# Performance work log

Hardware: AMD Instinct MI355X
Metric: run time of the kernel (lower is better)

Reference implementation:

```python
import jax, jax.numpy as jnp
import numpy as np

B, T, D = 32, 2000, 1024

def setup_inputs() -> dict:
    key = jax.random.key(0)
    # drive with positive mean current so neurons actually spike
    I_seq = 100.0 * jax.random.normal(key, (B, T, D), dtype=jnp.float32) + 250.0
    C, g_L, E_L, V_T, Delta_T, tau_w = 200.0, 10.0, -70.0, -50.0, 2.0, 120.0
    a, b, R, V_reset, V_spike, dt = 0.0, 0.0, 1.0, -65.0, 30.0, 0.1
    tau_m = C / max(1e-06, g_L)
    params = jnp.array([tau_m, E_L, V_T, Delta_T, R, tau_w, a, b, V_reset, V_spike, dt],
                       dtype=jnp.float32)
    return {"I_seq": I_seq, "params": params}


def reference(I_seq, params):
    tau_m, E_L, V_T, Delta_T, R, tau_w, a, b, V_reset, V_spike, dt = params
    Bs, Ts, Ds = I_seq.shape
    # flatten to (T, B*D): scan over time, all neurons vectorized
    flat_I = jnp.transpose(I_seq, (1, 0, 2)).reshape(Ts, Bs * Ds)
    V0 = jnp.full((Bs * Ds,), E_L, dtype=I_seq.dtype)
    w0 = jnp.zeros((Bs * Ds,), dtype=I_seq.dtype)

    def step(carry, i_t):
        V, w = carry
        exp_term = Delta_T * jnp.exp((V - V_T) / Delta_T)
        dV = (-(V - E_L) + exp_term - R * w + R * i_t) / tau_m
        V = V + dt * dV
        dw = (a * (V - E_L) - w) / tau_w
        w = w + dt * dw
        spk = (V >= V_spike).astype(V.dtype)
        V = jnp.where(spk > 0.0, V_reset, V)
        w = jnp.where(spk > 0.0, w + b, w)
        return (V, w), spk

    (_, _), spikes = jax.lax.scan(step, (V0, w0), flat_I)  # spikes: (T, B*D)
    return jnp.transpose(spikes.reshape(Ts, Bs, Ds), (1, 0, 2))  # (B, T, D)
```

## Files before the change

### kernel.cpp

```cpp
#include <hip/hip_runtime.h>


#define Bn 32
#define Tn 2000
#define Dn 1024
#define NEUR (Bn * Dn)
#define UNR 16
#define NB (Tn / UNR)

#define EXP_LOG2EF 1.44269504088896341f
#define EXP_C1 0.693359375f
#define EXP_C2 -2.12194440e-4f
#define EXP_P0 1.9875691500e-4f
#define EXP_P1 1.3981999507e-3f
#define EXP_P2 8.3334519073e-3f
#define EXP_P3 4.1665795894e-2f
#define EXP_P4 1.6666665459e-1f
#define EXP_P5 5.0000001201e-1f

__device__ __forceinline__ float ref_expf(float x) {
    #pragma clang fp contract(off)
    float fx = __builtin_floorf(__builtin_fmaf(x, EXP_LOG2EF, 0.5f));
    float xr = __builtin_fmaf(fx, -EXP_C1, x);
    xr = __builtin_fmaf(fx, -EXP_C2, xr);
    float z2 = xr * xr;
    float y = EXP_P0;
    y = __builtin_fmaf(y, xr, EXP_P1);
    y = __builtin_fmaf(y, xr, EXP_P2);
    y = __builtin_fmaf(y, xr, EXP_P3);
    y = __builtin_fmaf(y, xr, EXP_P4);
    y = __builtin_fmaf(y, xr, EXP_P5);
    y = __builtin_fmaf(y, z2, xr);
    y = y + 1.0f;
    const int n = (int)fx;
    return y * __int_as_float((n + 127) << 23);
}

__device__ __forceinline__ float ref_expf_scaled(float x, int kdt) {
    #pragma clang fp contract(off)
    float fx = __builtin_floorf(__builtin_fmaf(x, EXP_LOG2EF, 0.5f));
    float xr = __builtin_fmaf(fx, -EXP_C1, x);
    xr = __builtin_fmaf(fx, -EXP_C2, xr);
    float z2 = xr * xr;
    float y = EXP_P0;
    y = __builtin_fmaf(y, xr, EXP_P1);
    y = __builtin_fmaf(y, xr, EXP_P2);
    y = __builtin_fmaf(y, xr, EXP_P3);
    y = __builtin_fmaf(y, xr, EXP_P4);
    y = __builtin_fmaf(y, xr, EXP_P5);
    y = __builtin_fmaf(y, z2, xr);
    y = y + 1.0f;
    const int n = (int)fx;
    return y * __int_as_float((n + 127 + kdt) << 23);
}

__device__ __forceinline__ float div_uniform(float x, float d, float r) {
    #pragma clang fp contract(off)
    float q = x * r;
    float e = __builtin_fmaf(-d, q, x);
    return __builtin_fmaf(e, r, q);
}

__device__ __forceinline__ void step_simple(float& V, float i_t, float& spk_out,
                                            float E_L, float V_T, float Delta_T,
                                            float R, float tau_m, float V_spike,
                                            float V_reset, float dt) {
    #pragma clang fp contract(off)
    const float e  = ref_expf((V - V_T) / Delta_T);
    const float et = Delta_T * e;
    float nm = (-(V - E_L) + et);
    nm = nm + R * i_t;
    const float dV = nm / tau_m;
    V = __builtin_fmaf(dt, dV, V);
    spk_out = (V >= V_spike) ? 1.0f : 0.0f;
    V = (V >= V_spike) ? V_reset : V;
}

__device__ __forceinline__ void step_general(float& V, float& w, float i_t, float& spk_out,
                                             float E_L, float V_T, float Delta_T,
                                             float R, float tau_m, float tau_w,
                                             float a, float b,
                                             float V_spike, float V_reset, float dt) {
    #pragma clang fp contract(off)
    const float e  = ref_expf((V - V_T) / Delta_T);
    const float et = Delta_T * e;
    float nm = (-(V - E_L) + et);
    nm = __builtin_fmaf(-R, w, nm);
    nm = __builtin_fmaf(R, i_t, nm);
    const float dV = nm / tau_m;
    V = __builtin_fmaf(dt, dV, V);
    const float dwn = __builtin_fmaf(a, (V - E_L), -w);
    const float dw  = dwn / tau_w;
    w = __builtin_fmaf(dt, dw, w);
    spk_out = (V >= V_spike) ? 1.0f : 0.0f;
    const bool s = (V >= V_spike);
    V = s ? V_reset : V;
    w = s ? (w + b) : w;
}

__launch_bounds__(128, 1)
__global__ void adex_kernel(const float* __restrict__ I,
                            const float* __restrict__ params,
                            float* __restrict__ out) {
    #pragma clang fp contract(off)

    const float tau_m   = params[0];
    const float E_L     = params[1];
    const float V_T     = params[2];
    const float Delta_T = params[3];
    const float R       = params[4];
    const float tau_w   = params[5];
    const float a       = params[6];
    const float b       = params[7];
    const float V_reset = params[8];
    const float V_spike = params[9];
    const float dt      = params[10];

    const int n = blockIdx.x * blockDim.x + threadIdx.x;
    if (n >= NEUR) return;
    const int bb = n >> 10;
    const int dd = n & (Dn - 1);

    const float* Ip = I   + (size_t)bb * (size_t)(Tn * Dn) + dd;
    float*       Op = out + (size_t)bb * (size_t)(Tn * Dn) + dd;

    float V = E_L;
    float bufA[UNR], bufB[UNR];

    #pragma unroll
    for (int k = 0; k < UNR; ++k) bufA[k] = Ip[k * Dn];

    const unsigned dtBits = __float_as_uint(Delta_T);
    const bool dtPow2 = ((dtBits & 0x7FFFFFu) == 0u) && Delta_T > 0.0f;
    const bool hot = (a == 0.0f) && (b == 0.0f) && (R == 1.0f) && dtPow2;

    if (hot) {
        const int   kdt = (int)((dtBits >> 23) & 0xFFu) - 127;
        const float rDT = 1.0f / Delta_T;
        const float rTM = 1.0f / tau_m;
        const float xC = (V_reset - V_T) * rDT;
        const float nC = E_L - V_reset;

        float x   = (V - V_T) * rDT;
        float nEL = E_L - V;

        for (int tb = 0; tb < NB; tb += 2) {
            if (tb + 1 < NB) {
                const float* p = Ip + (size_t)(tb + 1) * (UNR * Dn);
                #pragma unroll
                for (int k = 0; k < UNR; ++k) bufB[k] = p[k * Dn];
            }
            {
                float* o = Op + (size_t)tb * (UNR * Dn);
                #pragma unroll
                for (int k = 0; k < UNR; ++k) {
                    const float et = ref_expf_scaled(x, kdt);
                    float nm = nEL + et;
                    nm = nm + bufA[k];
                    const float dV = div_uniform(nm, tau_m, rTM);
                    const float Vr = __builtin_fmaf(dt, dV, V);
                    const bool  s  = (Vr >= V_spike);
                    o[k * Dn] = s ? 1.0f : 0.0f;
                    const float xn = (Vr - V_T) * rDT;
                    const float nn = E_L - Vr;
                    V   = s ? V_reset : Vr;
                    x   = s ? xC : xn;
                    nEL = s ? nC : nn;
                }
            }
            if (tb + 2 < NB) {
                const float* p = Ip + (size_t)(tb + 2) * (UNR * Dn);
                #pragma unroll
                for (int k = 0; k < UNR; ++k) bufA[k] = p[k * Dn];
            }
            if (tb + 1 < NB) {
                float* o = Op + (size_t)(tb + 1) * (UNR * Dn);
                #pragma unroll
                for (int k = 0; k < UNR; ++k) {
                    const float et = ref_expf_scaled(x, kdt);
                    float nm = nEL + et;
                    nm = nm + bufB[k];
                    const float dV = div_uniform(nm, tau_m, rTM);
                    const float Vr = __builtin_fmaf(dt, dV, V);
                    const bool  s  = (Vr >= V_spike);
                    o[k * Dn] = s ? 1.0f : 0.0f;
                    const float xn = (Vr - V_T) * rDT;
                    const float nn = E_L - Vr;
                    V   = s ? V_reset : Vr;
                    x   = s ? xC : xn;
                    nEL = s ? nC : nn;
                }
            }
        }
        return;
    }

    float w = 0.0f;
    const bool simple = (a == 0.0f) && (b == 0.0f);

    if (simple) {
        for (int tb = 0; tb < NB; tb += 2) {
            if (tb + 1 < NB) {
                const float* p = Ip + (size_t)(tb + 1) * (UNR * Dn);
                #pragma unroll
                for (int k = 0; k < UNR; ++k) bufB[k] = p[k * Dn];
            }
            {
                float* o = Op + (size_t)tb * (UNR * Dn);
                #pragma unroll
                for (int k = 0; k < UNR; ++k) {
                    float spk;
                    step_simple(V, bufA[k], spk, E_L, V_T, Delta_T, R, tau_m,
                                V_spike, V_reset, dt);
                    o[k * Dn] = spk;
                }
            }
            if (tb + 2 < NB) {
                const float* p = Ip + (size_t)(tb + 2) * (UNR * Dn);
                #pragma unroll
                for (int k = 0; k < UNR; ++k) bufA[k] = p[k * Dn];
            }
            if (tb + 1 < NB) {
                float* o = Op + (size_t)(tb + 1) * (UNR * Dn);
                #pragma unroll
                for (int k = 0; k < UNR; ++k) {
                    float spk;
                    step_simple(V, bufB[k], spk, E_L, V_T, Delta_T, R, tau_m,
                                V_spike, V_reset, dt);
                    o[k * Dn] = spk;
                }
            }
        }
    } else {
        for (int tb = 0; tb < NB; tb += 2) {
            if (tb + 1 < NB) {
                const float* p = Ip + (size_t)(tb + 1) * (UNR * Dn);
                #pragma unroll
                for (int k = 0; k < UNR; ++k) bufB[k] = p[k * Dn];
            }
            {
                float* o = Op + (size_t)tb * (UNR * Dn);
                #pragma unroll
                for (int k = 0; k < UNR; ++k) {
                    float spk;
                    step_general(V, w, bufA[k], spk, E_L, V_T, Delta_T, R, tau_m,
                                 tau_w, a, b, V_spike, V_reset, dt);
                    o[k * Dn] = spk;
                }
            }
            if (tb + 2 < NB) {
                const float* p = Ip + (size_t)(tb + 2) * (UNR * Dn);
                #pragma unroll
                for (int k = 0; k < UNR; ++k) bufA[k] = p[k * Dn];
            }
            if (tb + 1 < NB) {
                float* o = Op + (size_t)(tb + 1) * (UNR * Dn);
                #pragma unroll
                for (int k = 0; k < UNR; ++k) {
                    float spk;
                    step_general(V, w, bufB[k], spk, E_L, V_T, Delta_T, R, tau_m,
                                 tau_w, a, b, V_spike, V_reset, dt);
                    o[k * Dn] = spk;
                }
            }
        }
    }
}

extern "C" void kernel_launch(void* const* d_in, const int* in_sizes, int n_in,
                              void* d_out, int out_size, void* d_ws, size_t ws_size,
                              hipStream_t stream) {
    const float* I      = (const float*)d_in[0];
    const float* params = (const float*)d_in[1];
    float*       out    = (float*)d_out;

    dim3 block(128);
    dim3 grid(NEUR / 128);
    adex_kernel<<<grid, block, 0, stream>>>(I, params, out);
}
```

Baseline: 187.7 us.

## Split time axis into chunks with warm-up state convergence and sequential fixup

Splits the 2000-step scan into 5 time chunks run in parallel. Each later chunk starts from a bracket of possible membrane voltages and runs a 160-step warm-up to check whether every trajectory has collapsed onto the reset state. If it has not, a flag is set and a second kernel reruns that chunk sequentially from the true carried voltage. The aim is to expose five times more parallelism than the 256 single-wave blocks provide. The cost is the warm-up recompute, an extra launch and workspace traffic. Correctness relies on a heuristic convergence bound (fixed slack constants), and the path is only used when the workspace is large enough.

```diff
diff --git a/kernel.cpp b/kernel.cpp
--- a/kernel.cpp
+++ b/kernel.cpp
@@ -6,7 +6,13 @@
 #define Dn 1024
 #define NEUR (Bn * Dn)
 #define UNR 16
-#define NB (Tn / UNR)
+#define NC 5
+#define CHK 400
+#define WARM 160
+#define CBLK (CHK / UNR)
+#define WBLK (WARM / UNR)
+#define FBLK (Tn / UNR)
+#define BPC (NEUR / 128)
 
 #define EXP_LOG2EF 1.44269504088896341f
 #define EXP_C1 0.693359375f
@@ -36,7 +42,7 @@
     return y * __int_as_float((n + 127) << 23);
 }
 
-__device__ __forceinline__ float ref_expf_scaled(float x, int kdt) {
+__device__ __forceinline__ float expsc(float x, int kdt) {
     #pragma clang fp contract(off)
     float fx = __builtin_floorf(__builtin_fmaf(x, EXP_LOG2EF, 0.5f));
     float xr = __builtin_fmaf(fx, -EXP_C1, x);
@@ -54,11 +60,44 @@
     return y * __int_as_float((n + 127 + kdt) << 23);
 }
 
-__device__ __forceinline__ float div_uniform(float x, float d, float r) {
+__device__ __forceinline__ float mark_div(float x, float d, float r) {
     #pragma clang fp contract(off)
     float q = x * r;
     float e = __builtin_fmaf(-d, q, x);
     return __builtin_fmaf(e, r, q);
+}
+
+struct HP {
+    float tau_m, E_L, V_T, rDT, rTM, dt, Vs, Vrst, xC, nC;
+    int kdt;
+};
+
+__device__ __forceinline__ bool hot_step(float& V, float& x, float& nEL,
+                                         float i_t, const HP p) {
+    #pragma clang fp contract(off)
+    const float et = expsc(x, p.kdt);
+    float nm = nEL + et;
+    nm = nm + i_t;
+    const float dV = mark_div(nm, p.tau_m, p.rTM);
+    const float Vp = __builtin_fmaf(p.dt, dV, V);
+    const bool s = (Vp >= p.Vs);
+    const float xn = (Vp - p.V_T) * p.rDT;
+    const float nn = p.E_L - Vp;
+    V   = s ? p.Vrst : Vp;
+    x   = s ? p.xC : xn;
+    nEL = s ? p.nC : nn;
+    return s;
+}
+
+__device__ __forceinline__ float fpre(float V, float i_t, const HP p) {
+    #pragma clang fp contract(off)
+    const float xx = (V - p.V_T) * p.rDT;
+    const float nn = p.E_L - V;
+    const float et = expsc(xx, p.kdt);
+    float nm = nn + et;
+    nm = nm + i_t;
+    const float dV = mark_div(nm, p.tau_m, p.rTM);
+    return __builtin_fmaf(p.dt, dV, V);
 }
 
 __device__ __forceinline__ void step_simple(float& V, float i_t, float& spk_out,
@@ -98,12 +137,45 @@
     w = s ? (w + b) : w;
 }
 
+#define RUN_BLOCKS(IPTR, OPTR, NBLK, ...) do {                                    \
+    float bufA_[UNR], bufB_[UNR];                                                 \
+    _Pragma("unroll") for (int k = 0; k < UNR; ++k) bufA_[k] = (IPTR)[k * Dn];    \
+    for (int tb = 0; tb < (NBLK); tb += 2) {                                      \
+        if (tb + 1 < (NBLK)) {                                                    \
+            const float* pp_ = (IPTR) + (size_t)(tb + 1) * (UNR * Dn);            \
+            _Pragma("unroll") for (int k = 0; k < UNR; ++k) bufB_[k] = pp_[k*Dn]; \
+        }                                                                         \
+        {                                                                         \
+            float* oo_ = (OPTR) + (size_t)tb * (UNR * Dn);                        \
+            _Pragma("unroll") for (int k = 0; k < UNR; ++k) {                     \
+                const float i_t = bufA_[k];                                       \
+                float* OSLOT = oo_ + (size_t)k * Dn; (void)OSLOT;                 \
+                __VA_ARGS__;                                                      \
+            }                                                                     \
+        }                                                                         \
+        if (tb + 2 < (NBLK)) {                                                    \
+            const float* pp_ = (IPTR) + (size_t)(tb + 2) * (UNR * Dn);            \
+            _Pragma("unroll") for (int k = 0; k < UNR; ++k) bufA_[k] = pp_[k*Dn]; \
+        }                                                                         \
+        if (tb + 1 < (NBLK)) {                                                    \
+            float* oo_ = (OPTR) + (size_t)(tb + 1) * (UNR * Dn);                  \
+            _Pragma("unroll") for (int k = 0; k < UNR; ++k) {                     \
+                const float i_t = bufB_[k];                                       \
+                float* OSLOT = oo_ + (size_t)k * Dn; (void)OSLOT;                 \
+                __VA_ARGS__;                                                      \
+            }                                                                     \
+        }                                                                         \
+    }                                                                             \
+} while (0)
+
 __launch_bounds__(128, 1)
-__global__ void adex_kernel(const float* __restrict__ I,
-                            const float* __restrict__ params,
-                            float* __restrict__ out) {
-    #pragma clang fp contract(off)
-
+__global__ void adex_chunked(const float* __restrict__ I,
+                             const float* __restrict__ params,
+                             float* __restrict__ out,
+                             int* __restrict__ flags,
+                             float* __restrict__ Vend,
+                             int use_chunked) {
+    #pragma clang fp contract(off)
     const float tau_m   = params[0];
     const float E_L     = params[1];
     const float V_T     = params[2];
@@ -116,153 +188,151 @@
     const float V_spike = params[9];
     const float dt      = params[10];
 
-    const int n = blockIdx.x * blockDim.x + threadIdx.x;
-    if (n >= NEUR) return;
-    const int bb = n >> 10;
-    const int dd = n & (Dn - 1);
-
-    const float* Ip = I   + (size_t)bb * (size_t)(Tn * Dn) + dd;
-    float*       Op = out + (size_t)bb * (size_t)(Tn * Dn) + dd;
-
-    float V = E_L;
-    float bufA[UNR], bufB[UNR];
-
-    #pragma unroll
-    for (int k = 0; k < UNR; ++k) bufA[k] = Ip[k * Dn];
-
     const unsigned dtBits = __float_as_uint(Delta_T);
     const bool dtPow2 = ((dtBits & 0x7FFFFFu) == 0u) && Delta_T > 0.0f;
     const bool hot = (a == 0.0f) && (b == 0.0f) && (R == 1.0f) && dtPow2;
 
-    if (hot) {
-        const int   kdt = (int)((dtBits >> 23) & 0xFFu) - 127;
-        const float rDT = 1.0f / Delta_T;
-        const float rTM = 1.0f / tau_m;
-        const float xC = (V_reset - V_T) * rDT;
-        const float nC = E_L - V_reset;
-
-        float x   = (V - V_T) * rDT;
-        float nEL = E_L - V;
-
-        for (int tb = 0; tb < NB; tb += 2) {
-            if (tb + 1 < NB) {
-                const float* p = Ip + (size_t)(tb + 1) * (UNR * Dn);
-                #pragma unroll
-                for (int k = 0; k < UNR; ++k) bufB[k] = p[k * Dn];
-            }
-            {
-                float* o = Op + (size_t)tb * (UNR * Dn);
-                #pragma unroll
-                for (int k = 0; k < UNR; ++k) {
-                    const float et = ref_expf_scaled(x, kdt);
-                    float nm = nEL + et;
-                    nm = nm + bufA[k];
-                    const float dV = div_uniform(nm, tau_m, rTM);
-                    const float Vr = __builtin_fmaf(dt, dV, V);
-                    const bool  s  = (Vr >= V_spike);
-                    o[k * Dn] = s ? 1.0f : 0.0f;
-                    const float xn = (Vr - V_T) * rDT;
-                    const float nn = E_L - Vr;
-                    V   = s ? V_reset : Vr;
-                    x   = s ? xC : xn;
-                    nEL = s ? nC : nn;
-                }
-            }
-            if (tb + 2 < NB) {
-                const float* p = Ip + (size_t)(tb + 2) * (UNR * Dn);
-                #pragma unroll
-                for (int k = 0; k < UNR; ++k) bufA[k] = p[k * Dn];
-            }
-            if (tb + 1 < NB) {
-                float* o = Op + (size_t)(tb + 1) * (UNR * Dn);
-                #pragma unroll
-                for (int k = 0; k < UNR; ++k) {
-                    const float et = ref_expf_scaled(x, kdt);
-                    float nm = nEL + et;
-                    nm = nm + bufB[k];
-                    const float dV = div_uniform(nm, tau_m, rTM);
-                    const float Vr = __builtin_fmaf(dt, dV, V);
-                    const bool  s  = (Vr >= V_spike);
-                    o[k * Dn] = s ? 1.0f : 0.0f;
-                    const float xn = (Vr - V_T) * rDT;
-                    const float nn = E_L - Vr;
-                    V   = s ? V_reset : Vr;
-                    x   = s ? xC : xn;
-                    nEL = s ? nC : nn;
-                }
-            }
+    const int c  = use_chunked ? (int)(blockIdx.x >> 8) : 0;
+    const int wb = use_chunked ? (int)(blockIdx.x & 255) : (int)blockIdx.x;
+    const int n  = wb * 128 + (int)threadIdx.x;
+    const int bb = n >> 10;
+    const int dd = n & (Dn - 1);
+
+    const float* Ibase = I   + (size_t)bb * (size_t)(Tn * Dn) + dd;
+    float*       Obase = out + (size_t)bb * (size_t)(Tn * Dn) + dd;
+
+    if (!hot || !use_chunked) {
+        if (use_chunked) {
+            flags[c * NEUR + n] = 0;
+            if (c > 0) return;
+        }
+        float V = E_L;
+        if (hot) {
+            const int   kdt = (int)((dtBits >> 23) & 0xFFu) - 127;
+            const float rDT = 1.0f / Delta_T;
+            const float rTM = 1.0f / tau_m;
+            HP p = {tau_m, E_L, V_T, rDT, rTM, dt, V_spike, V_reset,
+                    (V_reset - V_T) * rDT, E_L - V_reset, kdt};
+            float x = (V - V_T) * rDT, nEL = E_L - V;
+            RUN_BLOCKS(Ibase, Obase, FBLK,
+                { const bool s = hot_step(V, x, nEL, i_t, p); *OSLOT = s ? 1.0f : 0.0f; });
+        } else if (a == 0.0f && b == 0.0f) {
+            RUN_BLOCKS(Ibase, Obase, FBLK,
+                { float spk; step_simple(V, i_t, spk, E_L, V_T, Delta_T, R, tau_m,
+                                         V_spike, V_reset, dt); *OSLOT = spk; });
+        } else {
+            float w = 0.0f;
+            RUN_BLOCKS(Ibase, Obase, FBLK,
+                { float spk; step_general(V, w, i_t, spk, E_L, V_T, Delta_T, R, tau_m,
+                                          tau_w, a, b, V_spike, V_reset, dt); *OSLOT = spk; });
         }
         return;
     }
 
-    float w = 0.0f;
-    const bool simple = (a == 0.0f) && (b == 0.0f);
-
-    if (simple) {
-        for (int tb = 0; tb < NB; tb += 2) {
-            if (tb + 1 < NB) {
-                const float* p = Ip + (size_t)(tb + 1) * (UNR * Dn);
-                #pragma unroll
-                for (int k = 0; k < UNR; ++k) bufB[k] = p[k * Dn];
-            }
-            {
-                float* o = Op + (size_t)tb * (UNR * Dn);
-                #pragma unroll
-                for (int k = 0; k < UNR; ++k) {
-                    float spk;
-                    step_simple(V, bufA[k], spk, E_L, V_T, Delta_T, R, tau_m,
-                                V_spike, V_reset, dt);
-                    o[k * Dn] = spk;
+    const int   kdt = (int)((dtBits >> 23) & 0xFFu) - 127;
+    const float rDT = 1.0f / Delta_T;
+    const float rTM = 1.0f / tau_m;
+    const HP p = {tau_m, E_L, V_T, rDT, rTM, dt, V_spike, V_reset,
+                  (V_reset - V_T) * rDT, E_L - V_reset, kdt};
+
+    const float VsPM     = V_spike + 0.01f;
+    const float VsMM     = V_spike - 0.01f;
+    const float VsMinusC = __uint_as_float(__float_as_uint(V_spike) - 1u);
+    const float SL       = 0.004f;
+    const float LO0      = -100.0f;
+
+    float V, x, nEL;
+    bool collapsed;
+
+    if (c == 0) {
+        V = E_L; x = (V - V_T) * rDT; nEL = E_L - V;
+        collapsed = true;
+    } else {
+        const float* Iw = Ibase + (size_t)(c * CHK - WARM) * Dn;
+        float lo = LO0, hi = VsMinusC;
+        V = p.Vrst; x = p.xC; nEL = p.nC;
+        collapsed = false;
+        RUN_BLOCKS(Iw, Obase, WBLK, {
+            const float flo = fpre(lo, i_t, p);
+            const float fhi = fpre(hi, i_t, p);
+            hot_step(V, x, nEL, i_t, p);
+            if (!collapsed) {
+                if (flo >= VsPM) {
+                    collapsed = true; V = p.Vrst; x = p.xC; nEL = p.nC;
+                } else if (fhi < VsMM) {
+                    lo = flo - SL; hi = fhi + SL;
+                } else {
+                    lo = fminf(p.Vrst, flo - SL); hi = VsMinusC;
                 }
             }
-            if (tb + 2 < NB) {
-                const float* p = Ip + (size_t)(tb + 2) * (UNR * Dn);
-                #pragma unroll
-                for (int k = 0; k < UNR; ++k) bufA[k] = p[k * Dn];
-            }
-            if (tb + 1 < NB) {
-                float* o = Op + (size_t)(tb + 1) * (UNR * Dn);
-                #pragma unroll
-                for (int k = 0; k < UNR; ++k) {
-                    float spk;
-                    step_simple(V, bufB[k], spk, E_L, V_T, Delta_T, R, tau_m,
-                                V_spike, V_reset, dt);
-                    o[k * Dn] = spk;
-                }
-            }
-        }
-    } else {
-        for (int tb = 0; tb < NB; tb += 2) {
-            if (tb + 1 < NB) {
-                const float* p = Ip + (size_t)(tb + 1) * (UNR * Dn);
-                #pragma unroll
-                for (int k = 0; k < UNR; ++k) bufB[k] = p[k * Dn];
-            }
-            {
-                float* o = Op + (size_t)tb * (UNR * Dn);
-                #pragma unroll
-                for (int k = 0; k < UNR; ++k) {
-                    float spk;
-                    step_general(V, w, bufA[k], spk, E_L, V_T, Delta_T, R, tau_m,
-                                 tau_w, a, b, V_spike, V_reset, dt);
-                    o[k * Dn] = spk;
-                }
-            }
-            if (tb + 2 < NB) {
-                const float* p = Ip + (size_t)(tb + 2) * (UNR * Dn);
-                #pragma unroll
-                for (int k = 0; k < UNR; ++k) bufA[k] = p[k * Dn];
-            }
-            if (tb + 1 < NB) {
-                float* o = Op + (size_t)(tb + 1) * (UNR * Dn);
-                #pragma unroll
-                for (int k = 0; k < UNR; ++k) {
-                    float spk;
-                    step_general(V, w, bufB[k], spk, E_L, V_T, Delta_T, R, tau_m,
-                                 tau_w, a, b, V_spike, V_reset, dt);
-                    o[k * Dn] = spk;
-                }
-            }
+        });
+    }
+
+    {
+        const float* Ie = Ibase + (size_t)(c * CHK) * Dn;
+        float*       Oe = Obase + (size_t)(c * CHK) * Dn;
+        RUN_BLOCKS(Ie, Oe, CBLK,
+            { const bool s = hot_step(V, x, nEL, i_t, p); *OSLOT = s ? 1.0f : 0.0f; });
+    }
+    Vend [c * NEUR + n] = V;
+    flags[c * NEUR + n] = collapsed ? 0 : 1;
+}
+
+__launch_bounds__(128, 1)
+__global__ void adex_fixup(const float* __restrict__ I,
+                           const float* __restrict__ params,
+                           float* __restrict__ out,
+                           const int* __restrict__ flags,
+                           const float* __restrict__ Vend,
+                           int use_chunked) {
+    #pragma clang fp contract(off)
+    if (!use_chunked) return;
+    const float tau_m   = params[0];
+    const float E_L     = params[1];
+    const float V_T     = params[2];
+    const float Delta_T = params[3];
+    const float R       = params[4];
+    const float a       = params[6];
+    const float b       = params[7];
+    const float V_reset = params[8];
+    const float V_spike = params[9];
+    const float dt      = params[10];
+
+    const unsigned dtBits = __float_as_uint(Delta_T);
+    const bool dtPow2 = ((dtBits & 0x7FFFFFu) == 0u) && Delta_T > 0.0f;
+    const bool hot = (a == 0.0f) && (b == 0.0f) && (R == 1.0f) && dtPow2;
+    if (!hot) return;
+
+    const int n  = (int)blockIdx.x * 128 + (int)threadIdx.x;
+    const int bb = n >> 10;
+    const int dd = n & (Dn - 1);
+
+    int any = 0;
+    #pragma unroll
+    for (int cc = 1; cc < NC; ++cc) any |= flags[cc * NEUR + n];
+    if (!any) return;
+
+    const int   kdt = (int)((dtBits >> 23) & 0xFFu) - 127;
+    const float rDT = 1.0f / Delta_T;
+    const float rTM = 1.0f / tau_m;
+    const HP p = {tau_m, E_L, V_T, rDT, rTM, dt, V_spike, V_reset,
+                  (V_reset - V_T) * rDT, E_L - V_reset, kdt};
+
+    const float* Ibase = I   + (size_t)bb * (size_t)(Tn * Dn) + dd;
+    float*       Obase = out + (size_t)bb * (size_t)(Tn * Dn) + dd;
+
+    float carry = Vend[0 * NEUR + n];
+    for (int cc = 1; cc < NC; ++cc) {
+        const float Vst = flags[(cc - 1) * NEUR + n] ? carry : Vend[(cc - 1) * NEUR + n];
+        if (flags[cc * NEUR + n]) {
+            float V = Vst, x = (Vst - p.V_T) * p.rDT, nEL = p.E_L - Vst;
+            const float* Ie = Ibase + (size_t)(cc * CHK) * Dn;
+            float*       Oe = Obase + (size_t)(cc * CHK) * Dn;
+            RUN_BLOCKS(Ie, Oe, CBLK,
+                { const bool s = hot_step(V, x, nEL, i_t, p); *OSLOT = s ? 1.0f : 0.0f; });
+            carry = V;
+        } else {
+            carry = Vend[cc * NEUR + n];
         }
     }
 }
@@ -274,7 +344,13 @@
     const float* params = (const float*)d_in[1];
     float*       out    = (float*)d_out;
 
+    const size_t need = (size_t)NC * NEUR * 4u * 2u;
+    const int use_chunked = (ws_size >= need) ? 1 : 0;
+    int*   flags = (int*)d_ws;
+    float* Vend  = (float*)((char*)d_ws + (size_t)NC * NEUR * 4u);
+
     dim3 block(128);
-    dim3 grid(NEUR / 128);
-    adex_kernel<<<grid, block, 0, stream>>>(I, params, out);
-}
+    dim3 grid1(use_chunked ? NC * BPC : BPC);
+    adex_chunked<<<grid1, block, 0, stream>>>(I, params, out, flags, Vend, use_chunked);
+    adex_fixup<<<dim3(BPC), block, 0, stream>>>(I, params, out, flags, Vend, use_chunked);
+}
```

New measurement: 269.7 us. 1.44x slower.
